# Kernel tuning notes

Hardware: AMD Instinct MI355X
Metric: run time of the kernel (lower is better)

## Reference

```python
import jax, jax.numpy as jnp
import numpy as np

NUM_TOKENS = 16384
INPUT_DIM = 4096
NUM_EXPERTS = 64
TOPK = 2


def setup_inputs() -> dict:
    key = jax.random.key(0)
    k1, k2 = jax.random.split(key)
    tokens = jax.random.normal(k1, (NUM_TOKENS, INPUT_DIM), dtype=jnp.float32)
    # nn.Linear(input_dim, num_experts).weight has shape [num_experts, input_dim]
    W = jax.random.normal(k2, (NUM_EXPERTS, INPUT_DIM), dtype=jnp.float32) * (1.0 / np.sqrt(INPUT_DIM))
    return {"tokens": tokens, "W": W}


def reference(tokens, W):
    # logits: [num_tokens, num_experts] = tokens @ W.T
    logits = jnp.einsum("td,ed->te", tokens, W)
    scores = jax.nn.softmax(logits, axis=-1)
    topk_scores, topk_indices = jax.lax.top_k(scores, TOPK)
    return topk_scores, topk_indices
```

## Files before the change

kernel.cpp:

```cpp
#include <hip/hip_runtime.h>
#include <math.h>

#define NTOK 16384
#define DIM  4096
#define NEXP 64
#define KS   4
#define KSL  (DIM / KS)
#define BK   32
#define NCH  (KSL / BK)
#define BM   64

typedef __fp16 f16x8  __attribute__((ext_vector_type(8)));
typedef __fp16 f16x2  __attribute__((ext_vector_type(2)));
typedef float  f32x16 __attribute__((ext_vector_type(16)));

__device__ __forceinline__ void gl_lds16(const void* g, void* l) {
  __builtin_amdgcn_global_load_lds(
      (const __attribute__((address_space(1))) void*)g,
      (__attribute__((address_space(3))) void*)l, 16, 0, 0);
}

__global__ __launch_bounds__(256) void split_w(
    const float* __restrict__ W,
    __fp16* __restrict__ Wh,
    __fp16* __restrict__ Wl)
{
  const int i = blockIdx.x * 256 + threadIdx.x;
  const float w = W[i];
  const __fp16 h = (__fp16)w;
  const float r = w - (float)h;
  Wh[i] = h;
  Wl[i] = (__fp16)r;
}

__global__ __launch_bounds__(256, 4) void router_mfma(
    const float* __restrict__ tokens,
    const __fp16* __restrict__ Wh,
    const __fp16* __restrict__ Wl,
    float* __restrict__ partial)
{
  __shared__ float  As[2][BM * BK];
  __shared__ __fp16 Bh[2][NEXP * BK];
  __shared__ __fp16 Bl[2][NEXP * BK];

  const int tid  = threadIdx.x;
  const int wid  = tid >> 6;
  const int lane = tid & 63;
  const int rc2  = lane & 31;
  const int q2   = lane >> 5;
  const int wr   = wid >> 1;
  const int ec   = wid & 1;
  const int s    = blockIdx.x & (KS - 1);
  const int tb   = (blockIdx.x >> 2) * BM;
  const int kbase = s * KSL;

  const int a_tl = lane >> 3, a_j = lane & 7;
  const float* asrc0 = tokens + (size_t)(tb + 16 * wid + a_tl) * DIM + kbase
                       + ((a_j ^ a_tl) << 2);
  const float* asrc1 = asrc0 + (size_t)8 * DIM;
  const int b_el = lane >> 2, b_j = lane & 3;
  const size_t boff = (size_t)(16 * wid + b_el) * DIM + kbase
                      + ((b_j ^ (b_el & 3)) << 3);
  const __fp16* bsrc_h = Wh + boff;
  const __fp16* bsrc_l = Wl + boff;

#define STAGE(buf, c) {                                  \
    const int ko = (c) * BK;                             \
    gl_lds16(asrc0 + ko, &As[buf][(16 * wid) * 32]);     \
    gl_lds16(asrc1 + ko, &As[buf][(16 * wid + 8) * 32]); \
    gl_lds16(bsrc_h + ko, &Bh[buf][(16 * wid) * 32]);    \
    gl_lds16(bsrc_l + ko, &Bl[buf][(16 * wid) * 32]);    \
  }

  f32x16 acc = {0,0,0,0, 0,0,0,0, 0,0,0,0, 0,0,0,0};

  const int akey = rc2 & 7;
  const int bkey = rc2 & 3;
  const int Arow = (32 * wr + rc2) * 32;
  const int Brow = (32 * ec + rc2) * 32;

#define KSTEP(buf, kk) {                                                     \
    const int u0 = 4 * (kk) + 2 * q2;                                        \
    const float4 a0 = *(const float4*)(&As[buf][Arow + ((u0    ) ^ akey) * 4]); \
    const float4 a1 = *(const float4*)(&As[buf][Arow + ((u0 + 1) ^ akey) * 4]); \
    const int ub = ((2 * (kk) + q2) ^ bkey) * 8;                             \
    const f16x8 bhv = *(const f16x8*)(&Bh[buf][Brow + ub]);                  \
    const f16x8 blv = *(const f16x8*)(&Bl[buf][Brow + ub]);                  \
    const f16x2 h0 = __builtin_amdgcn_cvt_pkrtz(a0.x, a0.y);                 \
    const f16x2 h1 = __builtin_amdgcn_cvt_pkrtz(a0.z, a0.w);                 \
    const f16x2 h2 = __builtin_amdgcn_cvt_pkrtz(a1.x, a1.y);                 \
    const f16x2 h3 = __builtin_amdgcn_cvt_pkrtz(a1.z, a1.w);                 \
    const f16x2 m0 = __builtin_amdgcn_cvt_pkrtz(a0.x - (float)h0[0],         \
                                                a0.y - (float)h0[1]);        \
    const f16x2 m1 = __builtin_amdgcn_cvt_pkrtz(a0.z - (float)h1[0],         \
                                                a0.w - (float)h1[1]);        \
    const f16x2 m2 = __builtin_amdgcn_cvt_pkrtz(a1.x - (float)h2[0],         \
                                                a1.y - (float)h2[1]);        \
    const f16x2 m3 = __builtin_amdgcn_cvt_pkrtz(a1.z - (float)h3[0],         \
                                                a1.w - (float)h3[1]);        \
    const f16x8 Ah = {h0[0],h0[1],h1[0],h1[1],h2[0],h2[1],h3[0],h3[1]};      \
    const f16x8 Am = {m0[0],m0[1],m1[0],m1[1],m2[0],m2[1],m3[0],m3[1]};      \
    acc = __builtin_amdgcn_mfma_f32_32x32x16_f16(Ah, bhv, acc, 0, 0, 0);     \
    acc = __builtin_amdgcn_mfma_f32_32x32x16_f16(Ah, blv, acc, 0, 0, 0);     \
    acc = __builtin_amdgcn_mfma_f32_32x32x16_f16(Am, bhv, acc, 0, 0, 0);     \
  }

#define COMP(buf) { KSTEP(buf, 0); KSTEP(buf, 1); }

  STAGE(0, 0);
  __syncthreads();

  for (int c = 0; c < NCH; c += 2) {
    if (c + 1 < NCH) STAGE(1, c + 1);
    COMP(0);
    __syncthreads();
    if (c + 2 < NCH) STAGE(0, c + 2);
    COMP(1);
    __syncthreads();
  }
#undef STAGE
#undef COMP
#undef KSTEP

  float* P = partial + ((size_t)s * NTOK + tb + 32 * wr) * NEXP + 32 * ec;
  #pragma unroll
  for (int reg = 0; reg < 16; ++reg) {
    const int row = (reg & 3) + 8 * (reg >> 2) + 4 * q2;
    P[(size_t)row * NEXP + rc2] = acc[reg];
  }
}

__global__ __launch_bounds__(256) void router_finish(
    const float* __restrict__ partial,
    float* __restrict__ out)
{
  const int t = blockIdx.x * 256 + threadIdx.x;

  float l[NEXP];
  const float* p0 = partial + (size_t)t * NEXP;
  #pragma unroll
  for (int qq = 0; qq < 16; ++qq) {
    const float4 v = *(const float4*)(p0 + qq * 4);
    l[qq*4+0] = v.x; l[qq*4+1] = v.y; l[qq*4+2] = v.z; l[qq*4+3] = v.w;
  }
  #pragma unroll
  for (int s = 1; s < KS; ++s) {
    const float* p = partial + ((size_t)s * NTOK + t) * NEXP;
    #pragma unroll
    for (int qq = 0; qq < 16; ++qq) {
      const float4 v = *(const float4*)(p + qq * 4);
      l[qq*4+0] += v.x; l[qq*4+1] += v.y; l[qq*4+2] += v.z; l[qq*4+3] += v.w;
    }
  }

  float t1v = l[0]; int t1i = 0;
  float t2v = -INFINITY; int t2i = NEXP;
  #pragma unroll
  for (int e = 1; e < NEXP; ++e) {
    const float v = l[e];
    if (v > t1v) { t2v = t1v; t2i = t1i; t1v = v; t1i = e; }
    else if (v > t2v) { t2v = v; t2i = e; }
  }

  float ssum = 0.f;
  #pragma unroll
  for (int e = 0; e < NEXP; ++e) ssum += expf(l[e] - t1v);

  const float inv = 1.0f / ssum;
  out[t * 2 + 0] = inv;
  out[t * 2 + 1] = expf(t2v - t1v) * inv;
  out[2 * NTOK + t * 2 + 0] = (float)t1i;
  out[2 * NTOK + t * 2 + 1] = (float)t2i;
}

extern "C" void kernel_launch(void* const* d_in, const int* in_sizes, int n_in,
                              void* d_out, int out_size, void* d_ws, size_t ws_size,
                              hipStream_t stream) {
  const float* tokens = (const float*)d_in[0];
  const float* W      = (const float*)d_in[1];
  float* out          = (float*)d_out;

  __fp16* Wh = (__fp16*)d_ws;
  __fp16* Wl = Wh + (size_t)NEXP * DIM;
  float* partial = (float*)((char*)d_ws + (size_t)2 * NEXP * DIM * sizeof(__fp16));

  split_w<<<(NEXP * DIM) / 256, 256, 0, stream>>>(W, Wh, Wl);
  router_mfma<<<(NTOK / BM) * KS, 256, 0, stream>>>(tokens, Wh, Wl, partial);
  router_finish<<<NTOK / 256, 256, 0, stream>>>(partial, out);
}
```

Before: 83.73 us.

## Double token tile per block and have each wave cover all experts

Raises the token tile from 64 to 128 rows per block. Each wave now owns 32 token rows and computes both 32-expert halves with two accumulators, so each token's fp16 hi/lo split is converted once and reused for twice as many MFMAs. This removes the duplicated A-side conversion and LDS reads that came from splitting experts across waves, and halves how often W is staged per token. In exchange the block uses more LDS and registers, the occupancy hint drops from 4 to 2, and the grid has half as many blocks.

New measurement: 83.07 us. No clear change (-0.8%).

```diff
diff --git a/kernel.cpp b/kernel.cpp
--- a/kernel.cpp
+++ b/kernel.cpp
@@ -8,7 +8,7 @@
 #define KSL  (DIM / KS)
 #define BK   32
 #define NCH  (KSL / BK)
-#define BM   64
+#define BM   128
 
 typedef __fp16 f16x8  __attribute__((ext_vector_type(8)));
 typedef __fp16 f16x2  __attribute__((ext_vector_type(2)));
@@ -33,7 +33,7 @@
   Wl[i] = (__fp16)r;
 }
 
-__global__ __launch_bounds__(256, 4) void router_mfma(
+__global__ __launch_bounds__(256, 2) void router_mfma(
     const float* __restrict__ tokens,
     const __fp16* __restrict__ Wh,
     const __fp16* __restrict__ Wl,
@@ -48,44 +48,47 @@
   const int lane = tid & 63;
   const int rc2  = lane & 31;
   const int q2   = lane >> 5;
-  const int wr   = wid >> 1;
-  const int ec   = wid & 1;
   const int s    = blockIdx.x & (KS - 1);
   const int tb   = (blockIdx.x >> 2) * BM;
   const int kbase = s * KSL;
 
   const int a_tl = lane >> 3, a_j = lane & 7;
-  const float* asrc0 = tokens + (size_t)(tb + 16 * wid + a_tl) * DIM + kbase
-                       + ((a_j ^ a_tl) << 2);
-  const float* asrc1 = asrc0 + (size_t)8 * DIM;
+  const float* asrc = tokens + (size_t)(tb + 32 * wid + a_tl) * DIM + kbase
+                      + ((a_j ^ a_tl) << 2);
   const int b_el = lane >> 2, b_j = lane & 3;
   const size_t boff = (size_t)(16 * wid + b_el) * DIM + kbase
                       + ((b_j ^ (b_el & 3)) << 3);
   const __fp16* bsrc_h = Wh + boff;
   const __fp16* bsrc_l = Wl + boff;
 
-#define STAGE(buf, c) {                                  \
-    const int ko = (c) * BK;                             \
-    gl_lds16(asrc0 + ko, &As[buf][(16 * wid) * 32]);     \
-    gl_lds16(asrc1 + ko, &As[buf][(16 * wid + 8) * 32]); \
-    gl_lds16(bsrc_h + ko, &Bh[buf][(16 * wid) * 32]);    \
-    gl_lds16(bsrc_l + ko, &Bl[buf][(16 * wid) * 32]);    \
+#define STAGE(buf, c) {                                               \
+    const int ko = (c) * BK;                                          \
+    gl_lds16(asrc + ko,                  &As[buf][(32*wid     ) * 32]); \
+    gl_lds16(asrc + (size_t) 8*DIM + ko, &As[buf][(32*wid +  8) * 32]); \
+    gl_lds16(asrc + (size_t)16*DIM + ko, &As[buf][(32*wid + 16) * 32]); \
+    gl_lds16(asrc + (size_t)24*DIM + ko, &As[buf][(32*wid + 24) * 32]); \
+    gl_lds16(bsrc_h + ko, &Bh[buf][(16 * wid) * 32]);                 \
+    gl_lds16(bsrc_l + ko, &Bl[buf][(16 * wid) * 32]);                 \
   }
 
-  f32x16 acc = {0,0,0,0, 0,0,0,0, 0,0,0,0, 0,0,0,0};
+  f32x16 accE0 = {0,0,0,0, 0,0,0,0, 0,0,0,0, 0,0,0,0};
+  f32x16 accE1 = {0,0,0,0, 0,0,0,0, 0,0,0,0, 0,0,0,0};
 
   const int akey = rc2 & 7;
   const int bkey = rc2 & 3;
-  const int Arow = (32 * wr + rc2) * 32;
-  const int Brow = (32 * ec + rc2) * 32;
+  const int Arow = (32 * wid + rc2) * 32;
+  const int Brow0 = rc2 * 32;
+  const int Brow1 = (32 + rc2) * 32;
 
 #define KSTEP(buf, kk) {                                                     \
     const int u0 = 4 * (kk) + 2 * q2;                                        \
     const float4 a0 = *(const float4*)(&As[buf][Arow + ((u0    ) ^ akey) * 4]); \
     const float4 a1 = *(const float4*)(&As[buf][Arow + ((u0 + 1) ^ akey) * 4]); \
     const int ub = ((2 * (kk) + q2) ^ bkey) * 8;                             \
-    const f16x8 bhv = *(const f16x8*)(&Bh[buf][Brow + ub]);                  \
-    const f16x8 blv = *(const f16x8*)(&Bl[buf][Brow + ub]);                  \
+    const f16x8 bh0 = *(const f16x8*)(&Bh[buf][Brow0 + ub]);                 \
+    const f16x8 bl0 = *(const f16x8*)(&Bl[buf][Brow0 + ub]);                 \
+    const f16x8 bh1 = *(const f16x8*)(&Bh[buf][Brow1 + ub]);                 \
+    const f16x8 bl1 = *(const f16x8*)(&Bl[buf][Brow1 + ub]);                 \
     const f16x2 h0 = __builtin_amdgcn_cvt_pkrtz(a0.x, a0.y);                 \
     const f16x2 h1 = __builtin_amdgcn_cvt_pkrtz(a0.z, a0.w);                 \
     const f16x2 h2 = __builtin_amdgcn_cvt_pkrtz(a1.x, a1.y);                 \
@@ -100,9 +103,12 @@
                                                 a1.w - (float)h3[1]);        \
     const f16x8 Ah = {h0[0],h0[1],h1[0],h1[1],h2[0],h2[1],h3[0],h3[1]};      \
     const f16x8 Am = {m0[0],m0[1],m1[0],m1[1],m2[0],m2[1],m3[0],m3[1]};      \
-    acc = __builtin_amdgcn_mfma_f32_32x32x16_f16(Ah, bhv, acc, 0, 0, 0);     \
-    acc = __builtin_amdgcn_mfma_f32_32x32x16_f16(Ah, blv, acc, 0, 0, 0);     \
-    acc = __builtin_amdgcn_mfma_f32_32x32x16_f16(Am, bhv, acc, 0, 0, 0);     \
+    accE0 = __builtin_amdgcn_mfma_f32_32x32x16_f16(Ah, bh0, accE0, 0, 0, 0); \
+    accE1 = __builtin_amdgcn_mfma_f32_32x32x16_f16(Ah, bh1, accE1, 0, 0, 0); \
+    accE0 = __builtin_amdgcn_mfma_f32_32x32x16_f16(Ah, bl0, accE0, 0, 0, 0); \
+    accE1 = __builtin_amdgcn_mfma_f32_32x32x16_f16(Ah, bl1, accE1, 0, 0, 0); \
+    accE0 = __builtin_amdgcn_mfma_f32_32x32x16_f16(Am, bh0, accE0, 0, 0, 0); \
+    accE1 = __builtin_amdgcn_mfma_f32_32x32x16_f16(Am, bh1, accE1, 0, 0, 0); \
   }
 
 #define COMP(buf) { KSTEP(buf, 0); KSTEP(buf, 1); }
@@ -122,11 +128,12 @@
 #undef COMP
 #undef KSTEP
 
-  float* P = partial + ((size_t)s * NTOK + tb + 32 * wr) * NEXP + 32 * ec;
+  float* P = partial + ((size_t)s * NTOK + tb + 32 * wid) * NEXP;
   #pragma unroll
   for (int reg = 0; reg < 16; ++reg) {
     const int row = (reg & 3) + 8 * (reg >> 2) + 4 * q2;
-    P[(size_t)row * NEXP + rc2] = acc[reg];
+    P[(size_t)row * NEXP + rc2]      = accE0[reg];
+    P[(size_t)row * NEXP + 32 + rc2] = accE1[reg];
   }
 }
 
```

## Use 512-thread blocks with intra-block K split and wider K chunks

Applied to the files above, without the earlier changes.

Halves the grid-level K split and doubles the K chunk to 64. Each block now runs 8 waves, with two waves per output tile each handling half of every chunk, so LDS staging is shared across more waves. Each wave pair still writes separate partial sums, so the finish kernel still reduces four partials. LDS per block doubles and the larger block may limit occupancy, and the swizzle patterns change to match the wider rows.

Result: faster. 75.12 us (-10.3%).

```diff
diff --git a/kernel.cpp b/kernel.cpp
--- a/kernel.cpp
+++ b/kernel.cpp
@@ -4,11 +4,12 @@
 #define NTOK 16384
 #define DIM  4096
 #define NEXP 64
-#define KS   4
+#define KS   2
 #define KSL  (DIM / KS)
-#define BK   32
+#define BK   64
 #define NCH  (KSL / BK)
 #define BM   64
+#define KSF  4
 
 typedef __fp16 f16x8  __attribute__((ext_vector_type(8)));
 typedef __fp16 f16x2  __attribute__((ext_vector_type(2)));
@@ -33,7 +34,7 @@
   Wl[i] = (__fp16)r;
 }
 
-__global__ __launch_bounds__(256, 4) void router_mfma(
+__global__ __launch_bounds__(512, 2) void router_mfma(
     const float* __restrict__ tokens,
     const __fp16* __restrict__ Wh,
     const __fp16* __restrict__ Wl,
@@ -48,42 +49,47 @@
   const int lane = tid & 63;
   const int rc2  = lane & 31;
   const int q2   = lane >> 5;
-  const int wr   = wid >> 1;
-  const int ec   = wid & 1;
+  const int kh   = wid & 1;
+  const int ec   = (wid >> 1) & 1;
+  const int wr   = wid >> 2;
   const int s    = blockIdx.x & (KS - 1);
-  const int tb   = (blockIdx.x >> 2) * BM;
+  const int tb   = (blockIdx.x >> 1) * BM;
   const int kbase = s * KSL;
 
-  const int a_tl = lane >> 3, a_j = lane & 7;
-  const float* asrc0 = tokens + (size_t)(tb + 16 * wid + a_tl) * DIM + kbase
-                       + ((a_j ^ a_tl) << 2);
-  const float* asrc1 = asrc0 + (size_t)8 * DIM;
-  const int b_el = lane >> 2, b_j = lane & 3;
-  const size_t boff = (size_t)(16 * wid + b_el) * DIM + kbase
-                      + ((b_j ^ (b_el & 3)) << 3);
+  const int r4 = lane >> 4, aj = lane & 15;
+  const int ra0 = 8 * wid + r4;
+  const int ra1 = 8 * wid + 4 + r4;
+  const float* asrc0 = tokens + (size_t)(tb + ra0) * DIM + kbase
+                       + ((aj ^ (ra0 & 15)) << 2);
+  const float* asrc1 = tokens + (size_t)(tb + ra1) * DIM + kbase
+                       + ((aj ^ (ra1 & 15)) << 2);
+  const int e8 = lane >> 3, bj = lane & 7;
+  const int rb = 8 * wid + e8;
+  const size_t boff = (size_t)rb * DIM + kbase + ((bj ^ (rb & 7)) << 3);
   const __fp16* bsrc_h = Wh + boff;
   const __fp16* bsrc_l = Wl + boff;
 
-#define STAGE(buf, c) {                                  \
-    const int ko = (c) * BK;                             \
-    gl_lds16(asrc0 + ko, &As[buf][(16 * wid) * 32]);     \
-    gl_lds16(asrc1 + ko, &As[buf][(16 * wid + 8) * 32]); \
-    gl_lds16(bsrc_h + ko, &Bh[buf][(16 * wid) * 32]);    \
-    gl_lds16(bsrc_l + ko, &Bl[buf][(16 * wid) * 32]);    \
+#define STAGE(buf, c) {                                   \
+    const int ko = (c) * BK;                              \
+    gl_lds16(asrc0 + ko, &As[buf][(8 * wid) * BK]);       \
+    gl_lds16(asrc1 + ko, &As[buf][(8 * wid + 4) * BK]);   \
+    gl_lds16(bsrc_h + ko, &Bh[buf][(8 * wid) * BK]);      \
+    gl_lds16(bsrc_l + ko, &Bl[buf][(8 * wid) * BK]);      \
   }
 
   f32x16 acc = {0,0,0,0, 0,0,0,0, 0,0,0,0, 0,0,0,0};
 
-  const int akey = rc2 & 7;
-  const int bkey = rc2 & 3;
-  const int Arow = (32 * wr + rc2) * 32;
-  const int Brow = (32 * ec + rc2) * 32;
+  const int akey = rc2 & 15;
+  const int bkey = rc2 & 7;
+  const int Arow = (32 * wr + rc2) * BK;
+  const int Brow = (32 * ec + rc2) * BK;
 
 #define KSTEP(buf, kk) {                                                     \
-    const int u0 = 4 * (kk) + 2 * q2;                                        \
+    const int ks_ = 2 * kh + (kk);                                           \
+    const int u0 = 4 * ks_ + 2 * q2;                                         \
     const float4 a0 = *(const float4*)(&As[buf][Arow + ((u0    ) ^ akey) * 4]); \
     const float4 a1 = *(const float4*)(&As[buf][Arow + ((u0 + 1) ^ akey) * 4]); \
-    const int ub = ((2 * (kk) + q2) ^ bkey) * 8;                             \
+    const int ub = ((2 * ks_ + q2) ^ bkey) * 8;                              \
     const f16x8 bhv = *(const f16x8*)(&Bh[buf][Brow + ub]);                  \
     const f16x8 blv = *(const f16x8*)(&Bl[buf][Brow + ub]);                  \
     const f16x2 h0 = __builtin_amdgcn_cvt_pkrtz(a0.x, a0.y);                 \
@@ -122,7 +128,8 @@
 #undef COMP
 #undef KSTEP
 
-  float* P = partial + ((size_t)s * NTOK + tb + 32 * wr) * NEXP + 32 * ec;
+  float* P = partial + ((size_t)(2 * s + kh) * NTOK + tb + 32 * wr) * NEXP
+             + 32 * ec;
   #pragma unroll
   for (int reg = 0; reg < 16; ++reg) {
     const int row = (reg & 3) + 8 * (reg >> 2) + 4 * q2;
@@ -144,7 +151,7 @@
     l[qq*4+0] = v.x; l[qq*4+1] = v.y; l[qq*4+2] = v.z; l[qq*4+3] = v.w;
   }
   #pragma unroll
-  for (int s = 1; s < KS; ++s) {
+  for (int s = 1; s < KSF; ++s) {
     const float* p = partial + ((size_t)s * NTOK + t) * NEXP;
     #pragma unroll
     for (int qq = 0; qq < 16; ++qq) {
@@ -185,6 +192,6 @@
   float* partial = (float*)((char*)d_ws + (size_t)2 * NEXP * DIM * sizeof(__fp16));
 
   split_w<<<(NEXP * DIM) / 256, 256, 0, stream>>>(W, Wh, Wl);
-  router_mfma<<<(NTOK / BM) * KS, 256, 0, stream>>>(tokens, Wh, Wl, partial);
+  router_mfma<<<(NTOK / BM) * KS, 512, 0, stream>>>(tokens, Wh, Wl, partial);
   router_finish<<<NTOK / 256, 256, 0, stream>>>(partial, out);
 }
```
